# Performance work log

Hardware: AMD Instinct MI355X
Metric: run time of the kernel (lower is better)

## Reference

```python
import jax, jax.numpy as jnp
import numpy as np

E = 1024
H = 16
D = E // H  # head_dim = 64
B = 4
S = 2048


def setup_inputs() -> dict:
    key = jax.random.key(0)
    ks = jax.random.split(key, 10)
    sc = 1.0 / np.sqrt(E)
    return {
        "inputs": jax.random.normal(ks[0], (B, S, E), dtype=jnp.float32),
        "wq": jax.random.normal(ks[1], (E, E), dtype=jnp.float32) * sc,
        "bq": jnp.zeros((E,), dtype=jnp.float32),
        "wk": jax.random.normal(ks[2], (E, E), dtype=jnp.float32) * sc,
        "bk": jnp.zeros((E,), dtype=jnp.float32),
        "wv": jax.random.normal(ks[3], (E, E), dtype=jnp.float32) * sc,
        "bv": jnp.zeros((E,), dtype=jnp.float32),
        "wo": jax.random.normal(ks[4], (E, E), dtype=jnp.float32) * sc,
        "bo": jnp.zeros((E,), dtype=jnp.float32),
        "ln_gamma": jnp.ones((E,), dtype=jnp.float32),
        "ln_beta": jnp.zeros((E,), dtype=jnp.float32),
    }


def reference(inputs, wq, bq, wk, bk, wv, bv, wo, bo, ln_gamma, ln_beta):
    # QKV projections, split heads: [B,S,E] -> [B,H,S,D]
    def split_heads(x):
        return x.reshape(B, S, H, D).transpose(0, 2, 1, 3)

    q = split_heads(inputs @ wq + bq)
    k = split_heads(inputs @ wk + bk)
    v = split_heads(inputs @ wv + bv)

    scale = 1.0 / jnp.sqrt(jnp.asarray(D, dtype=inputs.dtype))
    score = jnp.einsum("bhqd,bhkd->bhqk", q, k) * scale  # [B,H,S,S]
    weights = jax.nn.softmax(score, axis=-1)
    out = jnp.einsum("bhqk,bhkd->bhqd", weights, v)  # [B,H,S,D]
    out = out.transpose(0, 2, 1, 3).reshape(B, S, E)
    out = out @ wo + bo

    # residual + LayerNorm(eps=1e-6)
    x = inputs + out
    mean = jnp.mean(x, axis=-1, keepdims=True)
    var = jnp.mean(jnp.square(x - mean), axis=-1, keepdims=True)
    x = (x - mean) * jax.lax.rsqrt(var + 1e-6)
    return x * ln_gamma + ln_beta
```

## Files before the change

### kernel.cpp

```cpp
#include <hip/hip_runtime.h>

#define E_DIM 1024
#define H_NUM 16
#define D_DIM 64
#define B_NUM 4
#define S_DIM 2048
#define M_DIM 8192

#define SCALE_Q 0.18033688011112042f
#define SMAX 10.0f

typedef _Float16 f16;
typedef __attribute__((ext_vector_type(4))) _Float16 f16x4;
typedef __attribute__((ext_vector_type(8))) _Float16 f16x8;
typedef __attribute__((ext_vector_type(2))) __fp16 h16x2;
typedef __attribute__((ext_vector_type(4))) float f32x4;

extern "C" __device__ float __ocml_native_exp2_f32(float);

#define MFMA32(a, b, c) __builtin_amdgcn_mfma_f32_16x16x32_f16(a, b, c, 0, 0, 0)

#define GLOBAL_LOAD_LDS_16(gp, lp)                                    \
  __builtin_amdgcn_global_load_lds(                                   \
      (const __attribute__((address_space(1))) void*)(gp),            \
      (__attribute__((address_space(3))) void*)(lp), 16, 0, 0)

__global__ __launch_bounds__(256) void k_convert_x(const float* __restrict__ x,
                                                   f16* __restrict__ xh) {
  size_t i = ((size_t)blockIdx.x * 256 + threadIdx.x) * 4;
  float4 v = *reinterpret_cast<const float4*>(x + i);
  f16x4 o = {(f16)v.x, (f16)v.y, (f16)v.z, (f16)v.w};
  *reinterpret_cast<f16x4*>(xh + i) = o;
}

__global__ __launch_bounds__(256) void k_transpose_w(
    const float* __restrict__ w0, const float* __restrict__ w1,
    const float* __restrict__ w2, const float* __restrict__ w3,
    f16* __restrict__ dst) {
  __shared__ float tile[32][33];
  const float* src = blockIdx.z == 0 ? w0 : blockIdx.z == 1 ? w1
                   : blockIdx.z == 2 ? w2 : w3;
  f16* out = dst + (size_t)blockIdx.z * (E_DIM * E_DIM);
  const int n0 = blockIdx.x * 32, k0 = blockIdx.y * 32;
  const int tx = threadIdx.x & 31, ty = threadIdx.x >> 5;
#pragma unroll
  for (int i = 0; i < 4; i++)
    tile[ty + i * 8][tx] = src[(size_t)(k0 + ty + i * 8) * E_DIM + n0 + tx];
  __syncthreads();
#pragma unroll
  for (int i = 0; i < 4; i++)
    out[(size_t)(n0 + ty + i * 8) * E_DIM + k0 + tx] = (f16)tile[tx][ty + i * 8];
}


#define NKT (E_DIM / 64)
#define SLOT_A (256 * 64)
#define SLOT_B (128 * 64)
#define GEMM_LDS_BYTES (3 * (SLOT_A + SLOT_B) * 2)

__device__ __forceinline__ void gemm_mainloop_v4(
    const f16* __restrict__ A, const f16* __restrict__ BT,
    int m0, int n0, short* smem, f32x4 (&acc)[4][4]) {
  short* Asb = smem;
  short* Bsb = smem + 3 * SLOT_A;
  const int t = threadIdx.x;
  const int wave = t >> 6, lane = t & 63;
  const int l15 = lane & 15, quad = lane >> 4;
  const int wm = (wave >> 1) * 64, wn = (wave & 1) * 64;
  const int tr = t >> 3, tc = t & 7;
  const int swz = (tc ^ (tr & 7)) * 8;
  const int el = tc * 8;

  const f16* gA[4];
  const f16* gB[2];
  int eoA[4], eoB[2];
#pragma unroll
  for (int i = 0; i < 4; i++) {
    gA[i] = A + (size_t)(m0 + i * 64 + tr) * E_DIM + swz;
    eoA[i] = (i * 64 + tr) * 64 + el;
  }
#pragma unroll
  for (int j = 0; j < 2; j++) {
    gB[j] = BT + (size_t)(n0 + j * 64 + tr) * E_DIM + swz;
    eoB[j] = (j * 64 + tr) * 64 + el;
  }

  auto stage = [&](int slot, int kt) {
    short* ab = Asb + slot * SLOT_A;
    short* bb = Bsb + slot * SLOT_B;
    const int k0 = kt * 64;
#pragma unroll
    for (int i = 0; i < 4; i++) GLOBAL_LOAD_LDS_16(gA[i] + k0, ab + eoA[i]);
#pragma unroll
    for (int j = 0; j < 2; j++) GLOBAL_LOAD_LDS_16(gB[j] + k0, bb + eoB[j]);
  };

  stage(0, 0);
  stage(1, 1);
  stage(2, 2);

  for (int kt = 0; kt < NKT; kt++) {
    if (kt == 0)
      asm volatile("s_waitcnt vmcnt(12)" ::: "memory");
    else if (kt < NKT - 1)
      asm volatile("s_waitcnt vmcnt(6)" ::: "memory");
    else
      asm volatile("s_waitcnt vmcnt(0)" ::: "memory");
    __builtin_amdgcn_s_barrier();
    if (kt >= 1 && kt + 2 < NKT) stage((kt + 2) % 3, kt + 2);

    const short* as = Asb + (kt % 3) * SLOT_A;
    const short* bs = Bsb + (kt % 3) * SLOT_B;
    f16x8 af[4][2], bf[4][2];
#pragma unroll
    for (int mf = 0; mf < 4; mf++)
#pragma unroll
      for (int ks = 0; ks < 2; ks++)
        af[mf][ks] = *reinterpret_cast<const f16x8*>(
            &as[(wm + mf * 16 + l15) * 64 + ((ks * 4 + quad) ^ (l15 & 7)) * 8]);
#pragma unroll
    for (int nf = 0; nf < 4; nf++)
#pragma unroll
      for (int ks = 0; ks < 2; ks++)
        bf[nf][ks] = *reinterpret_cast<const f16x8*>(
            &bs[(wn + nf * 16 + l15) * 64 + ((ks * 4 + quad) ^ (l15 & 7)) * 8]);

    __builtin_amdgcn_s_setprio(1);
#pragma unroll
    for (int mf = 0; mf < 4; mf++)
#pragma unroll
      for (int nf = 0; nf < 4; nf++) {
        acc[mf][nf] = MFMA32(af[mf][0], bf[nf][0], acc[mf][nf]);
        acc[mf][nf] = MFMA32(af[mf][1], bf[nf][1], acc[mf][nf]);
      }
    __builtin_amdgcn_s_setprio(0);
    asm volatile("s_waitcnt lgkmcnt(0)" ::: "memory");
  }
}

__global__ __launch_bounds__(512, 2) void k_gemm_qkv_v4(
    const f16* __restrict__ A, const f16* __restrict__ BT3,
    const float* __restrict__ bq, const float* __restrict__ bk,
    const float* __restrict__ bv, f16* __restrict__ Qb,
    f16* __restrict__ Kb, f16* __restrict__ VT) {
  extern __shared__ short smem[];
  const int xcd = blockIdx.x & 7;
  const int s = blockIdx.x >> 3;
  const int sr = s >> 5;
  const int r5 = s & 31;
  const int yt = xcd * 4 + (r5 >> 3);
  const int xt = sr * 8 + (r5 & 7);
  const int m0 = yt * 256, n0 = xt * 128;
  const int region = xt >> 3;
  const float* bias = region == 0 ? bq : region == 1 ? bk : bv;
  const float scale = region == 0 ? SCALE_Q : 1.0f;

  f32x4 acc[4][4] = {};
  gemm_mainloop_v4(A, BT3, m0, n0, smem, acc);

  const int t = threadIdx.x;
  const int wave = t >> 6, lane = t & 63;
  const int l15 = lane & 15, quad = lane >> 4;
  const int wm = (wave >> 1) * 64, wn = (wave & 1) * 64;
#pragma unroll
  for (int nf = 0; nf < 4; nf++) {
    const int col = (n0 + wn + nf * 16 + l15) & 1023;
    const float bv_ = bias[col];
    const int hh = col >> 6, dd = col & 63;
#pragma unroll
    for (int mf = 0; mf < 4; mf++) {
#pragma unroll
      for (int r = 0; r < 4; r++) {
        const int row = m0 + wm + mf * 16 + quad * 4 + r;
        const f16 v = (f16)((acc[mf][nf][r] + bv_) * scale);
        if (region == 0) {
          Qb[(size_t)row * E_DIM + col] = v;
        } else if (region == 1) {
          Kb[(size_t)row * E_DIM + col] = v;
        } else {
          const int bb = row >> 11, ss = row & 2047;
          VT[(((size_t)bb * H_NUM + hh) * D_DIM + dd) * S_DIM + ss] = v;
        }
      }
    }
  }
}

__global__ __launch_bounds__(512, 2) void k_gemm_o_v4(
    const f16* __restrict__ A, const f16* __restrict__ BT,
    const float* __restrict__ bias, f16* __restrict__ Cout) {
  extern __shared__ short smem[];
  const int xcd = blockIdx.x & 7;
  const int s = blockIdx.x >> 3;
  const int yt = xcd * 4 + (s >> 3);
  const int xt = s & 7;
  const int m0 = yt * 256, n0 = xt * 128;

  f32x4 acc[4][4] = {};
  gemm_mainloop_v4(A, BT, m0, n0, smem, acc);

  const int t = threadIdx.x;
  const int wave = t >> 6, lane = t & 63;
  const int l15 = lane & 15, quad = lane >> 4;
  const int wm = (wave >> 1) * 64, wn = (wave & 1) * 64;
#pragma unroll
  for (int nf = 0; nf < 4; nf++) {
    const int col = n0 + wn + nf * 16 + l15;
    const float bv = bias[col];
#pragma unroll
    for (int mf = 0; mf < 4; mf++) {
#pragma unroll
      for (int r = 0; r < 4; r++) {
        const int row = m0 + wm + mf * 16 + quad * 4 + r;
        Cout[(size_t)row * E_DIM + col] = (f16)(acc[mf][nf][r] + bv);
      }
    }
  }
}

__global__ __launch_bounds__(256, 4) void k_attention(
    const f16* __restrict__ Q, const f16* __restrict__ K,
    const f16* __restrict__ VT, f16* __restrict__ O) {
  __shared__ short Ks[2][64 * 64];
  __shared__ short Vs[2][64 * 64];
  const int bh = blockIdx.x, qt = blockIdx.y;
  const int b = bh >> 4, h = bh & 15;
  const int t = threadIdx.x;
  const int wave = t >> 6, lane = t & 63, l15 = lane & 15, quad = lane >> 4;
  const size_t rowbase = (size_t)b * S_DIM;
  const int ch = h * D_DIM;
  const int qb = qt * 128 + wave * 32;

  f16x8 qf[2][2];
#pragma unroll
  for (int g = 0; g < 2; g++) {
    const size_t qrow = rowbase + qb + g * 16 + l15;
    qf[g][0] = *reinterpret_cast<const f16x8*>(Q + qrow * E_DIM + ch + quad * 8);
    qf[g][1] = *reinterpret_cast<const f16x8*>(Q + qrow * E_DIM + ch + 32 + quad * 8);
  }

  f32x4 o_acc[2][4] = {};
  f32x4 l_acc[2] = {};
  const f16x8 ones8 = {(f16)1.f, (f16)1.f, (f16)1.f, (f16)1.f,
                       (f16)1.f, (f16)1.f, (f16)1.f, (f16)1.f};
  const f32x4 cinit = {-SMAX, -SMAX, -SMAX, -SMAX};

  const int cgp = lane & 7;
  const f16* vtb = VT + ((size_t)(b * H_NUM + h) * D_DIM) * S_DIM;
  const f16* kgp[2];
  const f16* vgp[2];
  int ofs[2];
#pragma unroll
  for (int i = 0; i < 2; i++) {
    const int slot = wave * 16 + i * 8 + (lane >> 3);
    const int nt = slot >> 4, qd = (slot >> 2) & 3, rr = slot & 3;
    const int p = (nt >> 1) * 32 + qd * 8 + (nt & 1) * 4 + rr;
    const int cgl = (cgp ^ (slot & 7)) * 8;
    kgp[i] = K + (rowbase + p) * E_DIM + ch + cgl;
    vgp[i] = vtb + (size_t)slot * S_DIM + cgl;
    ofs[i] = slot * 64 + cgp * 8;
  }

  auto issue = [&](int bf) {
#pragma unroll
    for (int i = 0; i < 2; i++) {
      GLOBAL_LOAD_LDS_16(kgp[i], &Ks[bf][ofs[i]]);
      GLOBAL_LOAD_LDS_16(vgp[i], &Vs[bf][ofs[i]]);
      kgp[i] += 64 * E_DIM;
      vgp[i] += 64;
    }
  };

  issue(0);

  for (int kt = 0; kt < S_DIM / 64; kt++) {
    __syncthreads();
    if (kt + 1 < S_DIM / 64) issue((kt + 1) & 1);
    const short* kb = &Ks[kt & 1][0];
    const short* vb = &Vs[kt & 1][0];

    f32x4 sacc[2][4];
    __builtin_amdgcn_s_setprio(1);
#pragma unroll
    for (int nt = 0; nt < 4; nt++) {
      f16x8 kf0 = *reinterpret_cast<const f16x8*>(
          &kb[(nt * 16 + l15) * 64 + (quad ^ (l15 & 7)) * 8]);
      f16x8 kf1 = *reinterpret_cast<const f16x8*>(
          &kb[(nt * 16 + l15) * 64 + ((4 | quad) ^ (l15 & 7)) * 8]);
#pragma unroll
      for (int g = 0; g < 2; g++) {
        sacc[g][nt] = MFMA32(kf0, qf[g][0], cinit);
        sacc[g][nt] = MFMA32(kf1, qf[g][1], sacc[g][nt]);
      }
    }
    __builtin_amdgcn_s_setprio(0);

    f16x8 a8[2][2];
#pragma unroll
    for (int g = 0; g < 2; g++)
#pragma unroll
      for (int kk = 0; kk < 2; kk++) {
        union { f16x8 v8; h16x2 h2[4]; } u;
#pragma unroll
        for (int half = 0; half < 2; half++) {
          const f32x4 s4 = sacc[g][kk * 2 + half];
          u.h2[half * 2 + 0] = __builtin_amdgcn_cvt_pkrtz(
              __ocml_native_exp2_f32(s4[0]), __ocml_native_exp2_f32(s4[1]));
          u.h2[half * 2 + 1] = __builtin_amdgcn_cvt_pkrtz(
              __ocml_native_exp2_f32(s4[2]), __ocml_native_exp2_f32(s4[3]));
        }
        a8[g][kk] = u.v8;
      }

    __builtin_amdgcn_s_setprio(1);
#pragma unroll
    for (int kk = 0; kk < 2; kk++) {
#pragma unroll
      for (int dt = 0; dt < 4; dt++) {
        f16x8 vf = *reinterpret_cast<const f16x8*>(
            &vb[(dt * 16 + l15) * 64 + ((kk * 4 + quad) ^ (l15 & 7)) * 8]);
#pragma unroll
        for (int g = 0; g < 2; g++)
          o_acc[g][dt] = MFMA32(a8[g][kk], vf, o_acc[g][dt]);
      }
#pragma unroll
      for (int g = 0; g < 2; g++)
        l_acc[g] = MFMA32(a8[g][kk], ones8, l_acc[g]);
    }
    __builtin_amdgcn_s_setprio(0);
  }

#pragma unroll
  for (int g = 0; g < 2; g++) {
    const size_t obase = rowbase + qb + g * 16;
#pragma unroll
    for (int r = 0; r < 4; r++) {
      const float rl = 1.0f / l_acc[g][r];
#pragma unroll
      for (int dt = 0; dt < 4; dt++) {
        float v = o_acc[g][dt][r] * rl;
        O[(obase + quad * 4 + r) * E_DIM + ch + dt * 16 + l15] = (f16)v;
      }
    }
  }
}

__global__ __launch_bounds__(256) void k_ln(
    const f16* __restrict__ proj, const float* __restrict__ x,
    const float* __restrict__ gamma, const float* __restrict__ beta,
    float* __restrict__ out) {
  const int row = blockIdx.x;
  const int t = threadIdx.x;
  const size_t base = (size_t)row * E_DIM + t * 4;
  f16x4 p = *reinterpret_cast<const f16x4*>(proj + base);
  float4 xi = *reinterpret_cast<const float4*>(x + base);
  float v0 = (float)p[0] + xi.x, v1 = (float)p[1] + xi.y;
  float v2 = (float)p[2] + xi.z, v3 = (float)p[3] + xi.w;
  float s1 = v0 + v1 + v2 + v3;
  float s2 = v0 * v0 + v1 * v1 + v2 * v2 + v3 * v3;
#pragma unroll
  for (int off = 1; off < 64; off <<= 1) {
    s1 += __shfl_xor(s1, off, 64);
    s2 += __shfl_xor(s2, off, 64);
  }
  __shared__ float sh1[4], sh2[4];
  const int wave = t >> 6;
  if ((t & 63) == 0) { sh1[wave] = s1; sh2[wave] = s2; }
  __syncthreads();
  s1 = sh1[0] + sh1[1] + sh1[2] + sh1[3];
  s2 = sh2[0] + sh2[1] + sh2[2] + sh2[3];
  const float mean = s1 * (1.0f / E_DIM);
  const float var = s2 * (1.0f / E_DIM) - mean * mean;
  const float rstd = rsqrtf(var + 1e-6f);
  float4 g = *reinterpret_cast<const float4*>(gamma + t * 4);
  float4 bb = *reinterpret_cast<const float4*>(beta + t * 4);
  float4 o;
  o.x = (v0 - mean) * rstd * g.x + bb.x;
  o.y = (v1 - mean) * rstd * g.y + bb.y;
  o.z = (v2 - mean) * rstd * g.z + bb.z;
  o.w = (v3 - mean) * rstd * g.w + bb.w;
  *reinterpret_cast<float4*>(out + base) = o;
}

extern "C" void kernel_launch(void* const* d_in, const int* in_sizes, int n_in,
                              void* d_out, int out_size, void* d_ws, size_t ws_size,
                              hipStream_t stream) {
  const float* x     = (const float*)d_in[0];
  const float* wq    = (const float*)d_in[1];
  const float* bq    = (const float*)d_in[2];
  const float* wk    = (const float*)d_in[3];
  const float* bk    = (const float*)d_in[4];
  const float* wv    = (const float*)d_in[5];
  const float* bv    = (const float*)d_in[6];
  const float* wo    = (const float*)d_in[7];
  const float* bo    = (const float*)d_in[8];
  const float* gamma = (const float*)d_in[9];
  const float* beta  = (const float*)d_in[10];

  char* ws = (char*)d_ws;
  const size_t MB = 1ull << 20;
  f16* wt   = (f16*)(ws + 0 * MB);
  f16* wot  = (f16*)(ws + 6 * MB);
  f16* xh   = (f16*)(ws + 8 * MB);
  f16* Qb   = (f16*)(ws + 24 * MB);
  f16* Kb   = (f16*)(ws + 40 * MB);
  f16* VTb  = (f16*)(ws + 56 * MB);
  f16* Ob   = (f16*)(ws + 72 * MB);
  f16* proj = (f16*)(ws + 24 * MB);

  static int attr_set = 0;
  if (!attr_set) {
    hipFuncSetAttribute((const void*)k_gemm_qkv_v4,
                        hipFuncAttributeMaxDynamicSharedMemorySize, GEMM_LDS_BYTES);
    hipFuncSetAttribute((const void*)k_gemm_o_v4,
                        hipFuncAttributeMaxDynamicSharedMemorySize, GEMM_LDS_BYTES);
    attr_set = 1;
  }

  k_convert_x<<<M_DIM * E_DIM / 4 / 256, 256, 0, stream>>>(x, xh);
  k_transpose_w<<<dim3(32, 32, 4), 256, 0, stream>>>(wq, wk, wv, wo, wt);
  k_gemm_qkv_v4<<<768, 512, GEMM_LDS_BYTES, stream>>>(xh, wt, bq, bk, bv, Qb, Kb, VTb);
  k_attention<<<dim3(B_NUM * H_NUM, S_DIM / 128), 256, 0, stream>>>(Qb, Kb, VTb, Ob);
  k_gemm_o_v4<<<256, 512, GEMM_LDS_BYTES, stream>>>(Ob, wot, bo, proj);
  k_ln<<<M_DIM, 256, 0, stream>>>(proj, x, gamma, beta, (float*)d_out);
}
```

Before: 284.4 us.

## Split GEMM k-tile into two half-steps interleaving LDS reads, prefetch and MFMA

The GEMM main loop now processes each 64-wide k-tile in two 32-wide halves. Each half loads its fragments from LDS, issues part of the next global-to-LDS prefetch (A rows in the first half, the remaining A rows and B in the second), then runs the MFMAs. Extra barriers and sched_barriers enforce this ping-pong ordering. The aim is to spread the global load issue and LDS reads across the MFMA work and to halve fragment register pressure, at the cost of more barriers per tile and a more fragile hand-written vmcnt accounting.

```diff
diff --git a/kernel.cpp b/kernel.cpp
--- a/kernel.cpp
+++ b/kernel.cpp
@@ -58,7 +58,7 @@
 #define SLOT_B (128 * 64)
 #define GEMM_LDS_BYTES (3 * (SLOT_A + SLOT_B) * 2)
 
-__device__ __forceinline__ void gemm_mainloop_v4(
+__device__ __forceinline__ void gemm_mainloop_v5(
     const f16* __restrict__ A, const f16* __restrict__ BT,
     int m0, int n0, short* smem, f32x4 (&acc)[4][4]) {
   short* Asb = smem;
@@ -85,60 +85,84 @@
     eoB[j] = (j * 64 + tr) * 64 + el;
   }
 
-  auto stage = [&](int slot, int kt) {
+  auto stageA = [&](int slot, int kt) {
+    short* ab = Asb + slot * SLOT_A;
+    const int k0 = kt * 64;
+#pragma unroll
+    for (int i = 0; i < 3; i++) GLOBAL_LOAD_LDS_16(gA[i] + k0, ab + eoA[i]);
+  };
+  auto stageB = [&](int slot, int kt) {
     short* ab = Asb + slot * SLOT_A;
     short* bb = Bsb + slot * SLOT_B;
     const int k0 = kt * 64;
-#pragma unroll
-    for (int i = 0; i < 4; i++) GLOBAL_LOAD_LDS_16(gA[i] + k0, ab + eoA[i]);
+    GLOBAL_LOAD_LDS_16(gA[3] + k0, ab + eoA[3]);
 #pragma unroll
     for (int j = 0; j < 2; j++) GLOBAL_LOAD_LDS_16(gB[j] + k0, bb + eoB[j]);
   };
 
-  stage(0, 0);
-  stage(1, 1);
-  stage(2, 2);
-
+  stageA(0, 0); stageB(0, 0);
+  stageA(1, 1); stageB(1, 1);
+  asm volatile("s_waitcnt vmcnt(6)" ::: "memory");
+  __builtin_amdgcn_s_barrier();
+
+  int rsel = 0, wsel = 2;
   for (int kt = 0; kt < NKT; kt++) {
-    if (kt == 0)
-      asm volatile("s_waitcnt vmcnt(12)" ::: "memory");
-    else if (kt < NKT - 1)
+    const short* as = Asb + rsel * SLOT_A;
+    const short* bs = Bsb + rsel * SLOT_B;
+    f16x8 af[4], bf[4];
+
+#pragma unroll
+    for (int mf = 0; mf < 4; mf++)
+      af[mf] = *reinterpret_cast<const f16x8*>(
+          &as[(wm + mf * 16 + l15) * 64 + (quad ^ (l15 & 7)) * 8]);
+#pragma unroll
+    for (int nf = 0; nf < 4; nf++)
+      bf[nf] = *reinterpret_cast<const f16x8*>(
+          &bs[(wn + nf * 16 + l15) * 64 + (quad ^ (l15 & 7)) * 8]);
+    if (kt + 2 < NKT) stageA(wsel, kt + 2);
+    __builtin_amdgcn_s_barrier();
+    asm volatile("s_waitcnt lgkmcnt(0)" ::: "memory");
+    __builtin_amdgcn_sched_barrier(0);
+    __builtin_amdgcn_s_setprio(1);
+#pragma unroll
+    for (int mf = 0; mf < 4; mf++)
+#pragma unroll
+      for (int nf = 0; nf < 4; nf++)
+        acc[mf][nf] = MFMA32(af[mf], bf[nf], acc[mf][nf]);
+    __builtin_amdgcn_s_setprio(0);
+    __builtin_amdgcn_s_barrier();
+
+#pragma unroll
+    for (int mf = 0; mf < 4; mf++)
+      af[mf] = *reinterpret_cast<const f16x8*>(
+          &as[(wm + mf * 16 + l15) * 64 + ((4 | quad) ^ (l15 & 7)) * 8]);
+#pragma unroll
+    for (int nf = 0; nf < 4; nf++)
+      bf[nf] = *reinterpret_cast<const f16x8*>(
+          &bs[(wn + nf * 16 + l15) * 64 + ((4 | quad) ^ (l15 & 7)) * 8]);
+    if (kt + 2 < NKT) stageB(wsel, kt + 2);
+    __builtin_amdgcn_s_barrier();
+    asm volatile("s_waitcnt lgkmcnt(0)" ::: "memory");
+    __builtin_amdgcn_sched_barrier(0);
+    __builtin_amdgcn_s_setprio(1);
+#pragma unroll
+    for (int mf = 0; mf < 4; mf++)
+#pragma unroll
+      for (int nf = 0; nf < 4; nf++)
+        acc[mf][nf] = MFMA32(af[mf], bf[nf], acc[mf][nf]);
+    __builtin_amdgcn_s_setprio(0);
+    if (kt < NKT - 2)
       asm volatile("s_waitcnt vmcnt(6)" ::: "memory");
-    else
+    else if (kt == NKT - 2)
       asm volatile("s_waitcnt vmcnt(0)" ::: "memory");
     __builtin_amdgcn_s_barrier();
-    if (kt >= 1 && kt + 2 < NKT) stage((kt + 2) % 3, kt + 2);
-
-    const short* as = Asb + (kt % 3) * SLOT_A;
-    const short* bs = Bsb + (kt % 3) * SLOT_B;
-    f16x8 af[4][2], bf[4][2];
-#pragma unroll
-    for (int mf = 0; mf < 4; mf++)
-#pragma unroll
-      for (int ks = 0; ks < 2; ks++)
-        af[mf][ks] = *reinterpret_cast<const f16x8*>(
-            &as[(wm + mf * 16 + l15) * 64 + ((ks * 4 + quad) ^ (l15 & 7)) * 8]);
-#pragma unroll
-    for (int nf = 0; nf < 4; nf++)
-#pragma unroll
-      for (int ks = 0; ks < 2; ks++)
-        bf[nf][ks] = *reinterpret_cast<const f16x8*>(
-            &bs[(wn + nf * 16 + l15) * 64 + ((ks * 4 + quad) ^ (l15 & 7)) * 8]);
-
-    __builtin_amdgcn_s_setprio(1);
-#pragma unroll
-    for (int mf = 0; mf < 4; mf++)
-#pragma unroll
-      for (int nf = 0; nf < 4; nf++) {
-        acc[mf][nf] = MFMA32(af[mf][0], bf[nf][0], acc[mf][nf]);
-        acc[mf][nf] = MFMA32(af[mf][1], bf[nf][1], acc[mf][nf]);
-      }
-    __builtin_amdgcn_s_setprio(0);
-    asm volatile("s_waitcnt lgkmcnt(0)" ::: "memory");
-  }
-}
-
-__global__ __launch_bounds__(512, 2) void k_gemm_qkv_v4(
+
+    rsel = rsel == 2 ? 0 : rsel + 1;
+    wsel = wsel == 2 ? 0 : wsel + 1;
+  }
+}
+
+__global__ __launch_bounds__(512, 2) void k_gemm_qkv_v5(
     const f16* __restrict__ A, const f16* __restrict__ BT3,
     const float* __restrict__ bq, const float* __restrict__ bk,
     const float* __restrict__ bv, f16* __restrict__ Qb,
@@ -156,7 +180,7 @@
   const float scale = region == 0 ? SCALE_Q : 1.0f;
 
   f32x4 acc[4][4] = {};
-  gemm_mainloop_v4(A, BT3, m0, n0, smem, acc);
+  gemm_mainloop_v5(A, BT3, m0, n0, smem, acc);
 
   const int t = threadIdx.x;
   const int wave = t >> 6, lane = t & 63;
@@ -186,7 +210,7 @@
   }
 }
 
-__global__ __launch_bounds__(512, 2) void k_gemm_o_v4(
+__global__ __launch_bounds__(512, 2) void k_gemm_o_v5(
     const f16* __restrict__ A, const f16* __restrict__ BT,
     const float* __restrict__ bias, f16* __restrict__ Cout) {
   extern __shared__ short smem[];
@@ -197,7 +221,7 @@
   const int m0 = yt * 256, n0 = xt * 128;
 
   f32x4 acc[4][4] = {};
-  gemm_mainloop_v4(A, BT, m0, n0, smem, acc);
+  gemm_mainloop_v5(A, BT, m0, n0, smem, acc);
 
   const int t = threadIdx.x;
   const int wave = t >> 6, lane = t & 63;
@@ -410,17 +434,17 @@
 
   static int attr_set = 0;
   if (!attr_set) {
-    hipFuncSetAttribute((const void*)k_gemm_qkv_v4,
+    hipFuncSetAttribute((const void*)k_gemm_qkv_v5,
                         hipFuncAttributeMaxDynamicSharedMemorySize, GEMM_LDS_BYTES);
-    hipFuncSetAttribute((const void*)k_gemm_o_v4,
+    hipFuncSetAttribute((const void*)k_gemm_o_v5,
                         hipFuncAttributeMaxDynamicSharedMemorySize, GEMM_LDS_BYTES);
     attr_set = 1;
   }
 
   k_convert_x<<<M_DIM * E_DIM / 4 / 256, 256, 0, stream>>>(x, xh);
   k_transpose_w<<<dim3(32, 32, 4), 256, 0, stream>>>(wq, wk, wv, wo, wt);
-  k_gemm_qkv_v4<<<768, 512, GEMM_LDS_BYTES, stream>>>(xh, wt, bq, bk, bv, Qb, Kb, VTb);
+  k_gemm_qkv_v5<<<768, 512, GEMM_LDS_BYTES, stream>>>(xh, wt, bq, bk, bv, Qb, Kb, VTb);
   k_attention<<<dim3(B_NUM * H_NUM, S_DIM / 128), 256, 0, stream>>>(Qb, Kb, VTb, Ob);
-  k_gemm_o_v4<<<256, 512, GEMM_LDS_BYTES, stream>>>(Ob, wot, bo, proj);
+  k_gemm_o_v5<<<256, 512, GEMM_LDS_BYTES, stream>>>(Ob, wot, bo, proj);
   k_ln<<<M_DIM, 256, 0, stream>>>(proj, x, gamma, beta, (float*)d_out);
 }
```

Result: no change. 285.1 us (+0.3%).

## Use 256x256 tiles with K=32 four-slot pipeline for QKV GEMM

Applied to the files above, without the earlier changes.

Replaces the QKV projection GEMM with a new kernel using 256x256 output tiles, a K step of 32 and a four-slot LDS ring with three stages in flight. The operand rows are packed so each 8-row LDS fragment carries two interleaved global rows, keeping MFMA inputs contiguous. The aim is higher data reuse and fewer global reads per FLOP. In exchange, each block needs 128KB of LDS and larger accumulator state, which limits occupancy and produces an uneven number of block waves. The O-projection GEMM is inlined unchanged.

```diff
diff --git a/kernel.cpp b/kernel.cpp
--- a/kernel.cpp
+++ b/kernel.cpp
@@ -53,16 +53,133 @@
 }
 
 
-#define NKT (E_DIM / 64)
-#define SLOT_A (256 * 64)
-#define SLOT_B (128 * 64)
-#define GEMM_LDS_BYTES (3 * (SLOT_A + SLOT_B) * 2)
-
-__device__ __forceinline__ void gemm_mainloop_v4(
+#define QUNIT_F16 16384
+#define QKV_LDS_BYTES (4 * QUNIT_F16 * 2)
+#define NU 32
+
+__global__ __launch_bounds__(512, 2) void k_gemm_qkv_v6(
+    const f16* __restrict__ A, const f16* __restrict__ BT3,
+    const float* __restrict__ bq, const float* __restrict__ bk,
+    const float* __restrict__ bv, f16* __restrict__ Qb,
+    f16* __restrict__ Kb, f16* __restrict__ VT) {
+  extern __shared__ short smem[];
+  const int xcd = blockIdx.x & 7;
+  const int s = blockIdx.x >> 3;
+  const int yt = xcd * 4 + (s & 3);
+  const int xt = s >> 2;
+  const int m0 = yt * 256, n0 = xt * 256;
+  const int region = xt >> 2;
+  const float* bias = region == 0 ? bq : region == 1 ? bk : bv;
+  const float scale = region == 0 ? SCALE_Q : 1.0f;
+
+  const int t = threadIdx.x;
+  const int wave = t >> 6, lane = t & 63;
+  const int l15 = lane & 15, quad = lane >> 4;
+  const int wr = wave >> 2, wc = wave & 3;
+
+  const int tr = t >> 3, tc = t & 7;
+  const int v = tc ^ (tr & 7);
+  const f16* srcA[2];
+  const f16* srcB[2];
+  int dofsA[2], dofsB[2];
+#pragma unroll
+  for (int i = 0; i < 2; i++) {
+    const int row = 128 * i + 2 * tr + (v >> 2);
+    const int kcol = (v & 3) * 8;
+    srcA[i] = A + (size_t)(m0 + row) * E_DIM + kcol;
+    srcB[i] = BT3 + (size_t)(n0 + row) * E_DIM + kcol;
+    dofsA[i] = (i * 512 + t) * 8;
+    dofsB[i] = 8192 + (i * 512 + t) * 8;
+  }
+  auto stage = [&](int u) {
+    short* ub = smem + (u & 3) * QUNIT_F16;
+    const int kb = u * 32;
+#pragma unroll
+    for (int i = 0; i < 2; i++) {
+      GLOBAL_LOAD_LDS_16(srcA[i] + kb, ub + dofsA[i]);
+      GLOBAL_LOAD_LDS_16(srcB[i] + kb, ub + dofsB[i]);
+    }
+  };
+
+  stage(0); stage(1); stage(2);
+
+  f32x4 acc[8][4] = {};
+  const int phalf = l15 >> 1;
+  const int slq = (((l15 & 1) * 4 + quad) ^ phalf) * 8;
+
+  for (int u = 0; u < NU; u++) {
+    if (u < NU - 2)
+      asm volatile("s_waitcnt vmcnt(8)" ::: "memory");
+    else if (u == NU - 2)
+      asm volatile("s_waitcnt vmcnt(4)" ::: "memory");
+    else
+      asm volatile("s_waitcnt vmcnt(0)" ::: "memory");
+    __builtin_amdgcn_s_barrier();
+    if (u + 3 < NU) stage(u + 3);
+
+    const short* ub = smem + (u & 3) * QUNIT_F16;
+    f16x8 af[8], bf[4];
+#pragma unroll
+    for (int mf = 0; mf < 8; mf++)
+      af[mf] = *reinterpret_cast<const f16x8*>(
+          &ub[(wr * 64 + mf * 8 + phalf) * 64 + slq]);
+#pragma unroll
+    for (int nf = 0; nf < 4; nf++)
+      bf[nf] = *reinterpret_cast<const f16x8*>(
+          &ub[8192 + (wc * 32 + nf * 8 + phalf) * 64 + slq]);
+
+    __builtin_amdgcn_s_setprio(1);
+#pragma unroll
+    for (int mf = 0; mf < 8; mf++)
+#pragma unroll
+      for (int nf = 0; nf < 4; nf++)
+        acc[mf][nf] = MFMA32(af[mf], bf[nf], acc[mf][nf]);
+    __builtin_amdgcn_s_setprio(0);
+    asm volatile("s_waitcnt lgkmcnt(0)" ::: "memory");
+  }
+
+#pragma unroll
+  for (int nf = 0; nf < 4; nf++) {
+    const int col = (n0 + wc * 64 + nf * 16 + l15) & 1023;
+    const float bv_ = bias[col];
+    const int hh = col >> 6, dd = col & 63;
+#pragma unroll
+    for (int mf = 0; mf < 8; mf++) {
+#pragma unroll
+      for (int r = 0; r < 4; r++) {
+        const int row = m0 + wr * 128 + mf * 16 + quad * 4 + r;
+        const f16 vv = (f16)((acc[mf][nf][r] + bv_) * scale);
+        if (region == 0) {
+          Qb[(size_t)row * E_DIM + col] = vv;
+        } else if (region == 1) {
+          Kb[(size_t)row * E_DIM + col] = vv;
+        } else {
+          const int bb = row >> 11, ss = row & 2047;
+          VT[(((size_t)bb * H_NUM + hh) * D_DIM + dd) * S_DIM + ss] = vv;
+        }
+      }
+    }
+  }
+}
+
+
+#define OSLOT_A (256 * 64)
+#define OSLOT_B (128 * 64)
+#define O_LDS_BYTES (3 * (OSLOT_A + OSLOT_B) * 2)
+#define ONKT (E_DIM / 64)
+
+__global__ __launch_bounds__(512, 2) void k_gemm_o_v4(
     const f16* __restrict__ A, const f16* __restrict__ BT,
-    int m0, int n0, short* smem, f32x4 (&acc)[4][4]) {
+    const float* __restrict__ bias, f16* __restrict__ Cout) {
+  extern __shared__ short smem[];
   short* Asb = smem;
-  short* Bsb = smem + 3 * SLOT_A;
+  short* Bsb = smem + 3 * OSLOT_A;
+  const int xcd = blockIdx.x & 7;
+  const int s = blockIdx.x >> 3;
+  const int yt = xcd * 4 + (s >> 3);
+  const int xt = s & 7;
+  const int m0 = yt * 256, n0 = xt * 128;
+
   const int t = threadIdx.x;
   const int wave = t >> 6, lane = t & 63;
   const int l15 = lane & 15, quad = lane >> 4;
@@ -84,10 +201,9 @@
     gB[j] = BT + (size_t)(n0 + j * 64 + tr) * E_DIM + swz;
     eoB[j] = (j * 64 + tr) * 64 + el;
   }
-
   auto stage = [&](int slot, int kt) {
-    short* ab = Asb + slot * SLOT_A;
-    short* bb = Bsb + slot * SLOT_B;
+    short* ab = Asb + slot * OSLOT_A;
+    short* bb = Bsb + slot * OSLOT_B;
     const int k0 = kt * 64;
 #pragma unroll
     for (int i = 0; i < 4; i++) GLOBAL_LOAD_LDS_16(gA[i] + k0, ab + eoA[i]);
@@ -95,22 +211,21 @@
     for (int j = 0; j < 2; j++) GLOBAL_LOAD_LDS_16(gB[j] + k0, bb + eoB[j]);
   };
 
-  stage(0, 0);
-  stage(1, 1);
-  stage(2, 2);
-
-  for (int kt = 0; kt < NKT; kt++) {
+  stage(0, 0); stage(1, 1); stage(2, 2);
+  f32x4 acc[4][4] = {};
+
+  for (int kt = 0; kt < ONKT; kt++) {
     if (kt == 0)
       asm volatile("s_waitcnt vmcnt(12)" ::: "memory");
-    else if (kt < NKT - 1)
+    else if (kt < ONKT - 1)
       asm volatile("s_waitcnt vmcnt(6)" ::: "memory");
     else
       asm volatile("s_waitcnt vmcnt(0)" ::: "memory");
     __builtin_amdgcn_s_barrier();
-    if (kt >= 1 && kt + 2 < NKT) stage((kt + 2) % 3, kt + 2);
-
-    const short* as = Asb + (kt % 3) * SLOT_A;
-    const short* bs = Bsb + (kt % 3) * SLOT_B;
+    if (kt >= 1 && kt + 2 < ONKT) stage((kt + 2) % 3, kt + 2);
+
+    const short* as = Asb + (kt % 3) * OSLOT_A;
+    const short* bs = Bsb + (kt % 3) * OSLOT_B;
     f16x8 af[4][2], bf[4][2];
 #pragma unroll
     for (int mf = 0; mf < 4; mf++)
@@ -136,73 +251,7 @@
     __builtin_amdgcn_s_setprio(0);
     asm volatile("s_waitcnt lgkmcnt(0)" ::: "memory");
   }
-}
-
-__global__ __launch_bounds__(512, 2) void k_gemm_qkv_v4(
-    const f16* __restrict__ A, const f16* __restrict__ BT3,
-    const float* __restrict__ bq, const float* __restrict__ bk,
-    const float* __restrict__ bv, f16* __restrict__ Qb,
-    f16* __restrict__ Kb, f16* __restrict__ VT) {
-  extern __shared__ short smem[];
-  const int xcd = blockIdx.x & 7;
-  const int s = blockIdx.x >> 3;
-  const int sr = s >> 5;
-  const int r5 = s & 31;
-  const int yt = xcd * 4 + (r5 >> 3);
-  const int xt = sr * 8 + (r5 & 7);
-  const int m0 = yt * 256, n0 = xt * 128;
-  const int region = xt >> 3;
-  const float* bias = region == 0 ? bq : region == 1 ? bk : bv;
-  const float scale = region == 0 ? SCALE_Q : 1.0f;
-
-  f32x4 acc[4][4] = {};
-  gemm_mainloop_v4(A, BT3, m0, n0, smem, acc);
-
-  const int t = threadIdx.x;
-  const int wave = t >> 6, lane = t & 63;
-  const int l15 = lane & 15, quad = lane >> 4;
-  const int wm = (wave >> 1) * 64, wn = (wave & 1) * 64;
-#pragma unroll
-  for (int nf = 0; nf < 4; nf++) {
-    const int col = (n0 + wn + nf * 16 + l15) & 1023;
-    const float bv_ = bias[col];
-    const int hh = col >> 6, dd = col & 63;
-#pragma unroll
-    for (int mf = 0; mf < 4; mf++) {
-#pragma unroll
-      for (int r = 0; r < 4; r++) {
-        const int row = m0 + wm + mf * 16 + quad * 4 + r;
-        const f16 v = (f16)((acc[mf][nf][r] + bv_) * scale);
-        if (region == 0) {
-          Qb[(size_t)row * E_DIM + col] = v;
-        } else if (region == 1) {
-          Kb[(size_t)row * E_DIM + col] = v;
-        } else {
-          const int bb = row >> 11, ss = row & 2047;
-          VT[(((size_t)bb * H_NUM + hh) * D_DIM + dd) * S_DIM + ss] = v;
-        }
-      }
-    }
-  }
-}
-
-__global__ __launch_bounds__(512, 2) void k_gemm_o_v4(
-    const f16* __restrict__ A, const f16* __restrict__ BT,
-    const float* __restrict__ bias, f16* __restrict__ Cout) {
-  extern __shared__ short smem[];
-  const int xcd = blockIdx.x & 7;
-  const int s = blockIdx.x >> 3;
-  const int yt = xcd * 4 + (s >> 3);
-  const int xt = s & 7;
-  const int m0 = yt * 256, n0 = xt * 128;
-
-  f32x4 acc[4][4] = {};
-  gemm_mainloop_v4(A, BT, m0, n0, smem, acc);
-
-  const int t = threadIdx.x;
-  const int wave = t >> 6, lane = t & 63;
-  const int l15 = lane & 15, quad = lane >> 4;
-  const int wm = (wave >> 1) * 64, wn = (wave & 1) * 64;
+
 #pragma unroll
   for (int nf = 0; nf < 4; nf++) {
     const int col = n0 + wn + nf * 16 + l15;
@@ -410,17 +459,17 @@
 
   static int attr_set = 0;
   if (!attr_set) {
-    hipFuncSetAttribute((const void*)k_gemm_qkv_v4,
-                        hipFuncAttributeMaxDynamicSharedMemorySize, GEMM_LDS_BYTES);
+    hipFuncSetAttribute((const void*)k_gemm_qkv_v6,
+                        hipFuncAttributeMaxDynamicSharedMemorySize, QKV_LDS_BYTES);
     hipFuncSetAttribute((const void*)k_gemm_o_v4,
-                        hipFuncAttributeMaxDynamicSharedMemorySize, GEMM_LDS_BYTES);
+                        hipFuncAttributeMaxDynamicSharedMemorySize, O_LDS_BYTES);
     attr_set = 1;
   }
 
   k_convert_x<<<M_DIM * E_DIM / 4 / 256, 256, 0, stream>>>(x, xh);
   k_transpose_w<<<dim3(32, 32, 4), 256, 0, stream>>>(wq, wk, wv, wo, wt);
-  k_gemm_qkv_v4<<<768, 512, GEMM_LDS_BYTES, stream>>>(xh, wt, bq, bk, bv, Qb, Kb, VTb);
+  k_gemm_qkv_v6<<<384, 512, QKV_LDS_BYTES, stream>>>(xh, wt, bq, bk, bv, Qb, Kb, VTb);
   k_attention<<<dim3(B_NUM * H_NUM, S_DIM / 128), 256, 0, stream>>>(Qb, Kb, VTb, Ob);
-  k_gemm_o_v4<<<256, 512, GEMM_LDS_BYTES, stream>>>(Ob, wot, bo, proj);
+  k_gemm_o_v4<<<256, 512, O_LDS_BYTES, stream>>>(Ob, wot, bo, proj);
   k_ln<<<M_DIM, 256, 0, stream>>>(proj, x, gamma, beta, (float*)d_out);
 }
```

After: 309.7 us. +8.9%, slower.

## Shrink GEMM tiles to 128x128 with k32 stages and higher occupancy

Applied to the files above, without the earlier changes.

Both projection GEMMs move from 256x128 tiles with 512 threads and 64-wide k stages to 128x128 tiles with 256 threads and 32-wide k stages. Each stage now packs two rows per 64-element LDS line with a new XOR swizzle, and LDS is statically sized at 48KB so three blocks can share a CU. The grid doubles in size with a remapped XCD-aware tile order. The aim is better occupancy and load balance across CUs, at the cost of less data reuse per block and more barriers per k step.

```diff
diff --git a/kernel.cpp b/kernel.cpp
--- a/kernel.cpp
+++ b/kernel.cpp
@@ -53,110 +53,97 @@
 }
 
 
-#define NKT (E_DIM / 64)
-#define SLOT_A (256 * 64)
-#define SLOT_B (128 * 64)
-#define GEMM_LDS_BYTES (3 * (SLOT_A + SLOT_B) * 2)
-
-__device__ __forceinline__ void gemm_mainloop_v4(
+#define NU 32
+#define UNIT_F16 8192
+
+__device__ __forceinline__ void gemm_mainloop_v8(
     const f16* __restrict__ A, const f16* __restrict__ BT,
     int m0, int n0, short* smem, f32x4 (&acc)[4][4]) {
-  short* Asb = smem;
-  short* Bsb = smem + 3 * SLOT_A;
   const int t = threadIdx.x;
   const int wave = t >> 6, lane = t & 63;
   const int l15 = lane & 15, quad = lane >> 4;
   const int wm = (wave >> 1) * 64, wn = (wave & 1) * 64;
-  const int tr = t >> 3, tc = t & 7;
-  const int swz = (tc ^ (tr & 7)) * 8;
-  const int el = tc * 8;
-
-  const f16* gA[4];
-  const f16* gB[2];
-  int eoA[4], eoB[2];
-#pragma unroll
-  for (int i = 0; i < 4; i++) {
-    gA[i] = A + (size_t)(m0 + i * 64 + tr) * E_DIM + swz;
-    eoA[i] = (i * 64 + tr) * 64 + el;
-  }
-#pragma unroll
-  for (int j = 0; j < 2; j++) {
-    gB[j] = BT + (size_t)(n0 + j * 64 + tr) * E_DIM + swz;
-    eoB[j] = (j * 64 + tr) * 64 + el;
-  }
-
-  auto stage = [&](int slot, int kt) {
-    short* ab = Asb + slot * SLOT_A;
-    short* bb = Bsb + slot * SLOT_B;
-    const int k0 = kt * 64;
-#pragma unroll
-    for (int i = 0; i < 4; i++) GLOBAL_LOAD_LDS_16(gA[i] + k0, ab + eoA[i]);
-#pragma unroll
-    for (int j = 0; j < 2; j++) GLOBAL_LOAD_LDS_16(gB[j] + k0, bb + eoB[j]);
+
+  const f16* srcA[2];
+  const f16* srcB[2];
+  int dofs[2];
+#pragma unroll
+  for (int i = 0; i < 2; i++) {
+    const int p = (t >> 3) + i * 32;
+    const int v = (t & 7) ^ (p & 7);
+    const int r = 2 * p + (v >> 2);
+    const int kg = v & 3;
+    srcA[i] = A + (size_t)(m0 + r) * E_DIM + kg * 8;
+    srcB[i] = BT + (size_t)(n0 + r) * E_DIM + kg * 8;
+    dofs[i] = t * 8 + i * 2048;
+  }
+  auto stage = [&](int u) {
+    short* ub = smem + (u % 3) * UNIT_F16;
+    const int kb = u * 32;
+#pragma unroll
+    for (int i = 0; i < 2; i++) {
+      GLOBAL_LOAD_LDS_16(srcA[i] + kb, ub + dofs[i]);
+      GLOBAL_LOAD_LDS_16(srcB[i] + kb, ub + 4096 + dofs[i]);
+    }
   };
 
-  stage(0, 0);
-  stage(1, 1);
-  stage(2, 2);
-
-  for (int kt = 0; kt < NKT; kt++) {
+  stage(0); stage(1); stage(2);
+
+  for (int kt = 0; kt < NU; kt++) {
     if (kt == 0)
-      asm volatile("s_waitcnt vmcnt(12)" ::: "memory");
-    else if (kt < NKT - 1)
-      asm volatile("s_waitcnt vmcnt(6)" ::: "memory");
+      asm volatile("s_waitcnt vmcnt(8)" ::: "memory");
+    else if (kt < NU - 1)
+      asm volatile("s_waitcnt vmcnt(4)" ::: "memory");
     else
       asm volatile("s_waitcnt vmcnt(0)" ::: "memory");
     __builtin_amdgcn_s_barrier();
-    if (kt >= 1 && kt + 2 < NKT) stage((kt + 2) % 3, kt + 2);
-
-    const short* as = Asb + (kt % 3) * SLOT_A;
-    const short* bs = Bsb + (kt % 3) * SLOT_B;
-    f16x8 af[4][2], bf[4][2];
+    if (kt >= 1 && kt + 2 < NU) stage(kt + 2);
+
+    const short* ub = smem + (kt % 3) * UNIT_F16;
+    f16x8 af[4], bf[4];
+#pragma unroll
+    for (int mf = 0; mf < 4; mf++) {
+      const int r = wm + mf * 16 + l15;
+      const int p = r >> 1;
+      af[mf] = *reinterpret_cast<const f16x8*>(
+          &ub[p * 64 + ((((r & 1) << 2) | quad) ^ (p & 7)) * 8]);
+    }
+#pragma unroll
+    for (int nf = 0; nf < 4; nf++) {
+      const int r = wn + nf * 16 + l15;
+      const int p = r >> 1;
+      bf[nf] = *reinterpret_cast<const f16x8*>(
+          &ub[4096 + p * 64 + ((((r & 1) << 2) | quad) ^ (p & 7)) * 8]);
+    }
+
+    __builtin_amdgcn_s_setprio(1);
 #pragma unroll
     for (int mf = 0; mf < 4; mf++)
 #pragma unroll
-      for (int ks = 0; ks < 2; ks++)
-        af[mf][ks] = *reinterpret_cast<const f16x8*>(
-            &as[(wm + mf * 16 + l15) * 64 + ((ks * 4 + quad) ^ (l15 & 7)) * 8]);
-#pragma unroll
-    for (int nf = 0; nf < 4; nf++)
-#pragma unroll
-      for (int ks = 0; ks < 2; ks++)
-        bf[nf][ks] = *reinterpret_cast<const f16x8*>(
-            &bs[(wn + nf * 16 + l15) * 64 + ((ks * 4 + quad) ^ (l15 & 7)) * 8]);
-
-    __builtin_amdgcn_s_setprio(1);
-#pragma unroll
-    for (int mf = 0; mf < 4; mf++)
-#pragma unroll
-      for (int nf = 0; nf < 4; nf++) {
-        acc[mf][nf] = MFMA32(af[mf][0], bf[nf][0], acc[mf][nf]);
-        acc[mf][nf] = MFMA32(af[mf][1], bf[nf][1], acc[mf][nf]);
-      }
+      for (int nf = 0; nf < 4; nf++)
+        acc[mf][nf] = MFMA32(af[mf], bf[nf], acc[mf][nf]);
     __builtin_amdgcn_s_setprio(0);
     asm volatile("s_waitcnt lgkmcnt(0)" ::: "memory");
   }
 }
 
-__global__ __launch_bounds__(512, 2) void k_gemm_qkv_v4(
+__global__ __launch_bounds__(256, 3) void k_gemm_qkv_v8(
     const f16* __restrict__ A, const f16* __restrict__ BT3,
     const float* __restrict__ bq, const float* __restrict__ bk,
     const float* __restrict__ bv, f16* __restrict__ Qb,
     f16* __restrict__ Kb, f16* __restrict__ VT) {
-  extern __shared__ short smem[];
+  __shared__ short smem[3 * UNIT_F16];
   const int xcd = blockIdx.x & 7;
   const int s = blockIdx.x >> 3;
-  const int sr = s >> 5;
-  const int r5 = s & 31;
-  const int yt = xcd * 4 + (r5 >> 3);
-  const int xt = sr * 8 + (r5 & 7);
-  const int m0 = yt * 256, n0 = xt * 128;
+  const int yt = xcd * 8 + ((s >> 3) & 7);
+  const int xt = (s & 7) | ((s >> 6) << 3);
+  const int m0 = yt * 128, n0 = xt * 128;
   const int region = xt >> 3;
   const float* bias = region == 0 ? bq : region == 1 ? bk : bv;
   const float scale = region == 0 ? SCALE_Q : 1.0f;
 
   f32x4 acc[4][4] = {};
-  gemm_mainloop_v4(A, BT3, m0, n0, smem, acc);
+  gemm_mainloop_v8(A, BT3, m0, n0, smem, acc);
 
   const int t = threadIdx.x;
   const int wave = t >> 6, lane = t & 63;
@@ -186,18 +173,18 @@
   }
 }
 
-__global__ __launch_bounds__(512, 2) void k_gemm_o_v4(
+__global__ __launch_bounds__(256, 3) void k_gemm_o_v8(
     const f16* __restrict__ A, const f16* __restrict__ BT,
     const float* __restrict__ bias, f16* __restrict__ Cout) {
-  extern __shared__ short smem[];
+  __shared__ short smem[3 * UNIT_F16];
   const int xcd = blockIdx.x & 7;
   const int s = blockIdx.x >> 3;
-  const int yt = xcd * 4 + (s >> 3);
+  const int yt = xcd * 8 + ((s >> 3) & 7);
   const int xt = s & 7;
-  const int m0 = yt * 256, n0 = xt * 128;
+  const int m0 = yt * 128, n0 = xt * 128;
 
   f32x4 acc[4][4] = {};
-  gemm_mainloop_v4(A, BT, m0, n0, smem, acc);
+  gemm_mainloop_v8(A, BT, m0, n0, smem, acc);
 
   const int t = threadIdx.x;
   const int wave = t >> 6, lane = t & 63;
@@ -408,19 +395,10 @@
   f16* Ob   = (f16*)(ws + 72 * MB);
   f16* proj = (f16*)(ws + 24 * MB);
 
-  static int attr_set = 0;
-  if (!attr_set) {
-    hipFuncSetAttribute((const void*)k_gemm_qkv_v4,
-                        hipFuncAttributeMaxDynamicSharedMemorySize, GEMM_LDS_BYTES);
-    hipFuncSetAttribute((const void*)k_gemm_o_v4,
-                        hipFuncAttributeMaxDynamicSharedMemorySize, GEMM_LDS_BYTES);
-    attr_set = 1;
-  }
-
   k_convert_x<<<M_DIM * E_DIM / 4 / 256, 256, 0, stream>>>(x, xh);
   k_transpose_w<<<dim3(32, 32, 4), 256, 0, stream>>>(wq, wk, wv, wo, wt);
-  k_gemm_qkv_v4<<<768, 512, GEMM_LDS_BYTES, stream>>>(xh, wt, bq, bk, bv, Qb, Kb, VTb);
+  k_gemm_qkv_v8<<<1536, 256, 0, stream>>>(xh, wt, bq, bk, bv, Qb, Kb, VTb);
   k_attention<<<dim3(B_NUM * H_NUM, S_DIM / 128), 256, 0, stream>>>(Qb, Kb, VTb, Ob);
-  k_gemm_o_v4<<<256, 512, GEMM_LDS_BYTES, stream>>>(Ob, wot, bo, proj);
+  k_gemm_o_v8<<<512, 256, 0, stream>>>(Ob, wot, bo, proj);
   k_ln<<<M_DIM, 256, 0, stream>>>(proj, x, gamma, beta, (float*)d_out);
 }
```

Result: no change. 286.4 us (+0.7%).
